# Optimization experiments

Hardware: AMD Instinct MI355X
Metric: run time of the kernel (lower is better)

## Reference

```python
import jax, jax.numpy as jnp
import numpy as np

N = 256
NH = 256  # GRU hidden units
K = 2     # local Hilbert space dim (hardcoded in module)


def gru_step(x, h, Wk, Wr, b):
    # TF keras GRU, reset_after=True, gate order (z, r, h)
    gx = x @ Wk + b[0]          # [B, 3*NH]
    gh = h @ Wr + b[1]          # [B, 3*NH]
    xz, xr, xh = jnp.split(gx, 3, axis=-1)
    hz, hr, hn = jnp.split(gh, 3, axis=-1)
    z = jax.nn.sigmoid(xz + hz)
    r = jax.nn.sigmoid(xr + hr)
    hh = jnp.tanh(xh + r * hn)
    return z * h + (1.0 - z) * hh


def setup_inputs() -> dict:
    key = jax.random.key(0)
    k1, k2, k3 = jax.random.split(key, 3)
    return {
        "gru_kernel": jax.random.normal(k1, (K, 3 * NH), jnp.float32) * 0.05,
        "gru_rec_kernel": jax.random.normal(k2, (NH, 3 * NH), jnp.float32) * 0.05,
        "gru_bias": jnp.zeros((2, 3 * NH), jnp.float32),
        "dense_kernel": jax.random.normal(k3, (NH, K), jnp.float32) * 0.05,
        "dense_bias": jnp.zeros((K,), jnp.float32),
        "nsamples": 2048,
    }


def reference(gru_kernel, gru_rec_kernel, gru_bias, dense_kernel, dense_bias, nsamples):
    keys = jax.random.split(jax.random.key(42), N)
    x0 = jnp.zeros((nsamples, K), jnp.float32)      # 0 * one_hot(0) == zeros
    h0 = jnp.zeros((nsamples, NH), jnp.float32)
    logP0 = jnp.zeros((nsamples,), jnp.float32)

    def step(carry, key):
        x, h, logP = carry
        h = gru_step(x, h, gru_kernel, gru_rec_kernel, gru_bias)
        probs = jax.nn.softmax(h @ dense_kernel + dense_bias, axis=-1)  # [B, K]
        log_probs = jnp.log(1e-10 + probs)
        s = jax.random.categorical(key, log_probs, axis=-1)             # [B]
        onehot = jax.nn.one_hot(s, K, dtype=jnp.float32)
        logP = logP + jnp.sum(log_probs * onehot, axis=1)
        return (onehot, h, logP), s

    (_, _, logP), samples = jax.lax.scan(step, (x0, h0, logP0), keys)
    samples = samples.T.astype(jnp.int32)  # [nsamples, N]
    return samples, logP
```

## Files before the change

### kernel.cpp

```cpp
#include <hip/hip_runtime.h>
#include <stdint.h>

#define NSTEPS 256
#define NHID   256
#define NG     768
#define BPB    8
#define TPB    768
#define NSAMP  2048

__device__ __forceinline__ uint32_t rotl32(uint32_t v, int r){ return (v<<r)|(v>>(32-r)); }

__device__ __forceinline__ void tf2x32(uint32_t k0, uint32_t k1,
                                       uint32_t x0, uint32_t x1,
                                       uint32_t& o0, uint32_t& o1){
  const uint32_t ks2 = k0 ^ k1 ^ 0x1BD11BDAu;
  x0 += k0; x1 += k1;
#define TF_R(r) { x0 += x1; x1 = rotl32(x1,(r)); x1 ^= x0; }
  TF_R(13) TF_R(15) TF_R(26) TF_R(6)
  x0 += k1;  x1 += ks2 + 1u;
  TF_R(17) TF_R(29) TF_R(16) TF_R(24)
  x0 += ks2; x1 += k0 + 2u;
  TF_R(13) TF_R(15) TF_R(26) TF_R(6)
  x0 += k0;  x1 += k1 + 3u;
  TF_R(17) TF_R(29) TF_R(16) TF_R(24)
  x0 += k1;  x1 += ks2 + 4u;
  TF_R(13) TF_R(15) TF_R(26) TF_R(6)
  x0 += ks2; x1 += k0 + 5u;
#undef TF_R
  o0 = x0; o1 = x1;
}

__device__ __forceinline__ float tanh_xla(float x){
  float xc = fminf(fmaxf(x, -9.0f), 9.0f);
  float x2 = xc*xc;
  float p = -2.76076847742355e-16f;
  p = fmaf(p, x2, 2.00018790482477e-13f);
  p = fmaf(p, x2, -8.60467152213735e-11f);
  p = fmaf(p, x2, 5.12229709037114e-08f);
  p = fmaf(p, x2, 1.48572235717979e-05f);
  p = fmaf(p, x2, 6.37261928875436e-04f);
  p = fmaf(p, x2, 4.89352455891786e-03f);
  p = p * xc;
  float q = 1.19825839466702e-06f;
  q = fmaf(q, x2, 1.18534705686654e-04f);
  q = fmaf(q, x2, 2.26843463243900e-03f);
  q = fmaf(q, x2, 4.89352518554385e-03f);
  float r = p / q;
  return (fabsf(x) < 0.0004f) ? x : r;
}

__device__ __forceinline__ float sigmoid_ref(float x){
  return fmaf(0.5f, tanh_xla(0.5f*x), 0.5f);
}

__device__ __forceinline__ void gfma(float4 h, float4 w0, float4 w1, float4 w2, float4 w3, float4& a){
  a.x = fmaf(h.x, w0.x, a.x); a.y = fmaf(h.x, w0.y, a.y);
  a.z = fmaf(h.x, w0.z, a.z); a.w = fmaf(h.x, w0.w, a.w);
  a.x = fmaf(h.y, w1.x, a.x); a.y = fmaf(h.y, w1.y, a.y);
  a.z = fmaf(h.y, w1.z, a.z); a.w = fmaf(h.y, w1.w, a.w);
  a.x = fmaf(h.z, w2.x, a.x); a.y = fmaf(h.z, w2.y, a.y);
  a.z = fmaf(h.z, w2.z, a.z); a.w = fmaf(h.z, w2.w, a.w);
  a.x = fmaf(h.w, w3.x, a.x); a.y = fmaf(h.w, w3.y, a.y);
  a.z = fmaf(h.w, w3.z, a.z); a.w = fmaf(h.w, w3.w, a.w);
}

__global__ __launch_bounds__(TPB, 3) void rnn_sampler(
    const float* __restrict__ Wk,
    const float* __restrict__ Wr,
    const float* __restrict__ Bias,
    const float* __restrict__ Dk,
    const float* __restrict__ Db,
    float* __restrict__ out)
{
  __shared__ float    h_lds[BPB][NHID];
  __shared__ float    part[4][BPB][NG];
  __shared__ uint32_t key0[NSTEPS];
  __shared__ uint32_t key1[NSTEPS];
  __shared__ float    wk_lds[2*NG];
  __shared__ float    bias_lds[2*NG];
  __shared__ float    dk_lds[NHID*2];
  __shared__ float    db_lds[2];
  __shared__ int      xsel[BPB];
  __shared__ float    logPs[BPB];

  const int tid  = threadIdx.x;
  const int b    = blockIdx.x;
  const int ks   = tid / 192;
  const int cq   = tid % 192;
  const int wid  = tid >> 6;
  const int lane = tid & 63;

  if (tid < NSTEPS) {
    uint32_t o0, o1;
    tf2x32(0u, 42u, 0u, (uint32_t)tid, o0, o1);
    key0[tid] = o0; key1[tid] = o1;
  }
  for (int i = tid; i < BPB*NHID; i += TPB) (&h_lds[0][0])[i] = 0.0f;
  for (int i = tid; i < 2*NG; i += TPB) { wk_lds[i] = Wk[i]; bias_lds[i] = Bias[i]; }
  for (int i = tid; i < NHID*2; i += TPB) dk_lds[i] = Dk[i];
  if (tid < 2) db_lds[tid] = Db[tid];
  if (tid < BPB) { xsel[tid] = 0; logPs[tid] = 0.0f; }
  __syncthreads();

  const int k0 = ks * 64;
  const float* wp = Wr + (size_t)k0 * NG + 4*cq;

  float4 acc[BPB];

  for (int t = 0; t <= NSTEPS; ++t) {
    if (t > 0 && wid < BPB) {
      const int tc = t - 1;
      const int s  = wid;
      float4 h4 = *(const float4*)&h_lds[s][lane * 4];
      float4 d0 = *(const float4*)&dk_lds[lane * 8];
      float4 d1 = *(const float4*)&dk_lds[lane * 8 + 4];
      float a0 = h4.x*d0.x + h4.y*d0.z + h4.z*d1.x + h4.w*d1.z;
      float a1 = h4.x*d0.y + h4.y*d0.w + h4.z*d1.y + h4.w*d1.w;
#pragma unroll
      for (int off = 32; off > 0; off >>= 1) {
        a0 += __shfl_down(a0, off);
        a1 += __shfl_down(a1, off);
      }
      float gv = 0.0f;
      if (lane < 2) {
        const int i = b * BPB + s;
        uint32_t o0, o1;
        tf2x32(key0[tc], key1[tc], 0u, (uint32_t)(2*i + lane), o0, o1);
        uint32_t bits = o0 ^ o1;
        const float TINY = 1.17549435e-38f;
        float u = __uint_as_float((bits >> 9) | 0x3f800000u) - 1.0f;
        u = fmaxf(TINY, u * (1.0f - TINY) + TINY);
        gv = -logf(-logf(u));
      }
      float g1 = __shfl(gv, 1);
      if (lane == 0) {
        float l0 = a0 + db_lds[0], l1 = a1 + db_lds[1];
        float m  = fmaxf(l0, l1);
        float e0 = expf(l0 - m), e1 = expf(l1 - m);
        float sum = e0 + e1;
        float p0 = e0 / sum, p1 = e1 / sum;
        float lp0 = logf(1e-10f + p0), lp1 = logf(1e-10f + p1);
        float v0 = gv + lp0, v1 = g1 + lp1;
        int st = (v1 > v0) ? 1 : 0;
        logPs[s] += st ? lp1 : lp0;
        xsel[s] = 1 + st;
        const int i = b * BPB + s;
        out[(size_t)i * NSTEPS + tc] = (float)st;
      }
    }
    if (t == NSTEPS) break;

#pragma unroll
    for (int s = 0; s < BPB; ++s) acc[s] = make_float4(0.f, 0.f, 0.f, 0.f);

#pragma unroll 2
    for (int g = 0; g < 16; ++g) {
      const float* rp = wp + (size_t)(4*g) * NG;
      float4 w0 = *(const float4*)(rp);
      float4 w1 = *(const float4*)(rp + NG);
      float4 w2 = *(const float4*)(rp + 2*NG);
      float4 w3 = *(const float4*)(rp + 3*NG);
#pragma unroll
      for (int s = 0; s < BPB; ++s) {
        float4 h4 = *(const float4*)&h_lds[s][k0 + 4*g];
        gfma(h4, w0, w1, w2, w3, acc[s]);
      }
    }

#pragma unroll
    for (int s = 0; s < BPB; ++s)
      *(float4*)&part[ks][s][4*cq] = acc[s];
    __syncthreads();

    if (tid < 512) {
      const int s = tid >> 6;
      const int n = (tid & 63) << 2;
      float4 pz0 = *(const float4*)&part[0][s][n];
      float4 pz2 = *(const float4*)&part[2][s][n];
      float4 pz1 = *(const float4*)&part[1][s][n];
      float4 pz3 = *(const float4*)&part[3][s][n];
      float4 pr0 = *(const float4*)&part[0][s][n+256];
      float4 pr2 = *(const float4*)&part[2][s][n+256];
      float4 pr1 = *(const float4*)&part[1][s][n+256];
      float4 pr3 = *(const float4*)&part[3][s][n+256];
      float4 pn0 = *(const float4*)&part[0][s][n+512];
      float4 pn2 = *(const float4*)&part[2][s][n+512];
      float4 pn1 = *(const float4*)&part[1][s][n+512];
      float4 pn3 = *(const float4*)&part[3][s][n+512];
      float4 bhz = *(const float4*)&bias_lds[NG + n];
      float4 bhr = *(const float4*)&bias_lds[NG + n + 256];
      float4 bhn = *(const float4*)&bias_lds[NG + n + 512];
      float4 gxz = *(const float4*)&bias_lds[n];
      float4 gxr = *(const float4*)&bias_lds[n + 256];
      float4 gxh = *(const float4*)&bias_lds[n + 512];
      const int xs = xsel[s];
      if (xs != 0) {
        const float* wkrow = wk_lds + (xs - 1) * NG;
        float4 w0 = *(const float4*)&wkrow[n];
        float4 w1 = *(const float4*)&wkrow[n + 256];
        float4 w2 = *(const float4*)&wkrow[n + 512];
        gxz.x = w0.x + gxz.x; gxz.y = w0.y + gxz.y; gxz.z = w0.z + gxz.z; gxz.w = w0.w + gxz.w;
        gxr.x = w1.x + gxr.x; gxr.y = w1.y + gxr.y; gxr.z = w1.z + gxr.z; gxr.w = w1.w + gxr.w;
        gxh.x = w2.x + gxh.x; gxh.y = w2.y + gxh.y; gxh.z = w2.z + gxh.z; gxh.w = w2.w + gxh.w;
      }
      float4 ho = *(const float4*)&h_lds[s][n];
      float4 hnew;
#define GCOMP(c) { \
      float ghz = ((pz0.c + pz2.c) + (pz1.c + pz3.c)) + bhz.c; \
      float ghr = ((pr0.c + pr2.c) + (pr1.c + pr3.c)) + bhr.c; \
      float ghn = ((pn0.c + pn2.c) + (pn1.c + pn3.c)) + bhn.c; \
      float zg = sigmoid_ref(gxz.c + ghz); \
      float rg = sigmoid_ref(gxr.c + ghr); \
      float hh = tanh_xla(gxh.c + rg * ghn); \
      hnew.c = zg * ho.c + (1.0f - zg) * hh; }
      GCOMP(x) GCOMP(y) GCOMP(z) GCOMP(w)
#undef GCOMP
      *(float4*)&h_lds[s][n] = hnew;
    }
    __syncthreads();
  }

  __syncthreads();

  if (tid < BPB) {
    const int i = b * BPB + tid;
    out[(size_t)NSAMP * NSTEPS + i] = logPs[tid];
  }
}

extern "C" void kernel_launch(void* const* d_in, const int* in_sizes, int n_in,
                              void* d_out, int out_size, void* d_ws, size_t ws_size,
                              hipStream_t stream) {
  const float* Wk = (const float*)d_in[0];
  const float* Wr = (const float*)d_in[1];
  const float* B  = (const float*)d_in[2];
  const float* Dk = (const float*)d_in[3];
  const float* Db = (const float*)d_in[4];
  float* out = (float*)d_out;
  rnn_sampler<<<dim3(NSAMP / BPB), dim3(TPB), 0, stream>>>(Wk, Wr, B, Dk, Db, out);
}
```

Measured before the change: 3.377 ms.

## Halve threads per block and give each thread eight output columns

Drops the block from 768 to 384 threads, so each thread now computes 8 gate columns instead of 4 for all 8 samples. Each h value read from LDS now feeds 8 FMAs, which raises register reuse and cuts LDS reads per FMA. The sampling head now runs on 6 wavefronts, two of which handle two samples each, and the gate update loops over the work in strides. The cost is more registers per thread (64 accumulators), fewer waves to hide the global weight loads, and launch_bounds has been removed.

New measurement: 4.439 ms. +31.5%, slower.

```diff
diff --git a/kernel.cpp b/kernel.cpp
--- a/kernel.cpp
+++ b/kernel.cpp
@@ -5,7 +5,7 @@
 #define NHID   256
 #define NG     768
 #define BPB    8
-#define TPB    768
+#define TPB    384
 #define NSAMP  2048
 
 __device__ __forceinline__ uint32_t rotl32(uint32_t v, int r){ return (v<<r)|(v>>(32-r)); }
@@ -53,18 +53,14 @@
   return fmaf(0.5f, tanh_xla(0.5f*x), 0.5f);
 }
 
-__device__ __forceinline__ void gfma(float4 h, float4 w0, float4 w1, float4 w2, float4 w3, float4& a){
-  a.x = fmaf(h.x, w0.x, a.x); a.y = fmaf(h.x, w0.y, a.y);
-  a.z = fmaf(h.x, w0.z, a.z); a.w = fmaf(h.x, w0.w, a.w);
-  a.x = fmaf(h.y, w1.x, a.x); a.y = fmaf(h.y, w1.y, a.y);
-  a.z = fmaf(h.y, w1.z, a.z); a.w = fmaf(h.y, w1.w, a.w);
-  a.x = fmaf(h.z, w2.x, a.x); a.y = fmaf(h.z, w2.y, a.y);
-  a.z = fmaf(h.z, w2.z, a.z); a.w = fmaf(h.z, w2.w, a.w);
-  a.x = fmaf(h.w, w3.x, a.x); a.y = fmaf(h.w, w3.y, a.y);
-  a.z = fmaf(h.w, w3.z, a.z); a.w = fmaf(h.w, w3.w, a.w);
-}
-
-__global__ __launch_bounds__(TPB, 3) void rnn_sampler(
+__device__ __forceinline__ void fma8(float hc, float4 wa, float4 wb, float4& a0, float4& a1){
+  a0.x = fmaf(hc, wa.x, a0.x); a0.y = fmaf(hc, wa.y, a0.y);
+  a0.z = fmaf(hc, wa.z, a0.z); a0.w = fmaf(hc, wa.w, a0.w);
+  a1.x = fmaf(hc, wb.x, a1.x); a1.y = fmaf(hc, wb.y, a1.y);
+  a1.z = fmaf(hc, wb.z, a1.z); a1.w = fmaf(hc, wb.w, a1.w);
+}
+
+__global__ void rnn_sampler(
     const float* __restrict__ Wk,
     const float* __restrict__ Wr,
     const float* __restrict__ Bias,
@@ -85,8 +81,8 @@
 
   const int tid  = threadIdx.x;
   const int b    = blockIdx.x;
-  const int ks   = tid / 192;
-  const int cq   = tid % 192;
+  const int ks   = tid / 96;
+  const int co   = tid % 96;
   const int wid  = tid >> 6;
   const int lane = tid & 63;
 
@@ -103,78 +99,94 @@
   __syncthreads();
 
   const int k0 = ks * 64;
-  const float* wp = Wr + (size_t)k0 * NG + 4*cq;
-
-  float4 acc[BPB];
+  const float* wp = Wr + (size_t)k0 * NG + 8*co;
+
+  float4 acc[BPB][2];
 
   for (int t = 0; t <= NSTEPS; ++t) {
-    if (t > 0 && wid < BPB) {
+    if (t > 0 && wid < 6) {
       const int tc = t - 1;
-      const int s  = wid;
-      float4 h4 = *(const float4*)&h_lds[s][lane * 4];
-      float4 d0 = *(const float4*)&dk_lds[lane * 8];
-      float4 d1 = *(const float4*)&dk_lds[lane * 8 + 4];
-      float a0 = h4.x*d0.x + h4.y*d0.z + h4.z*d1.x + h4.w*d1.z;
-      float a1 = h4.x*d0.y + h4.y*d0.w + h4.z*d1.y + h4.w*d1.w;
-#pragma unroll
-      for (int off = 32; off > 0; off >>= 1) {
-        a0 += __shfl_down(a0, off);
-        a1 += __shfl_down(a1, off);
+      const int nr = (wid < 4) ? 1 : 2;
+      for (int r = 0; r < nr; ++r) {
+        const int s = (r == 0) ? wid : wid + 2;
+        float4 h4 = *(const float4*)&h_lds[s][lane * 4];
+        float4 d0 = *(const float4*)&dk_lds[lane * 8];
+        float4 d1 = *(const float4*)&dk_lds[lane * 8 + 4];
+        float a0 = h4.x*d0.x + h4.y*d0.z + h4.z*d1.x + h4.w*d1.z;
+        float a1 = h4.x*d0.y + h4.y*d0.w + h4.z*d1.y + h4.w*d1.w;
+#pragma unroll
+        for (int off = 32; off > 0; off >>= 1) {
+          a0 += __shfl_down(a0, off);
+          a1 += __shfl_down(a1, off);
+        }
+        float gv = 0.0f;
+        if (lane < 2) {
+          const int i = b * BPB + s;
+          uint32_t o0, o1;
+          tf2x32(key0[tc], key1[tc], 0u, (uint32_t)(2*i + lane), o0, o1);
+          uint32_t bits = o0 ^ o1;
+          const float TINY = 1.17549435e-38f;
+          float u = __uint_as_float((bits >> 9) | 0x3f800000u) - 1.0f;
+          u = fmaxf(TINY, u * (1.0f - TINY) + TINY);
+          gv = -logf(-logf(u));
+        }
+        float g1 = __shfl(gv, 1);
+        if (lane == 0) {
+          float l0 = a0 + db_lds[0], l1 = a1 + db_lds[1];
+          float m  = fmaxf(l0, l1);
+          float e0 = expf(l0 - m), e1 = expf(l1 - m);
+          float sum = e0 + e1;
+          float p0 = e0 / sum, p1 = e1 / sum;
+          float lp0 = logf(1e-10f + p0), lp1 = logf(1e-10f + p1);
+          float v0 = gv + lp0, v1 = g1 + lp1;
+          int st = (v1 > v0) ? 1 : 0;
+          logPs[s] += st ? lp1 : lp0;
+          xsel[s] = 1 + st;
+          const int i = b * BPB + s;
+          out[(size_t)i * NSTEPS + tc] = (float)st;
+        }
       }
-      float gv = 0.0f;
-      if (lane < 2) {
-        const int i = b * BPB + s;
-        uint32_t o0, o1;
-        tf2x32(key0[tc], key1[tc], 0u, (uint32_t)(2*i + lane), o0, o1);
-        uint32_t bits = o0 ^ o1;
-        const float TINY = 1.17549435e-38f;
-        float u = __uint_as_float((bits >> 9) | 0x3f800000u) - 1.0f;
-        u = fmaxf(TINY, u * (1.0f - TINY) + TINY);
-        gv = -logf(-logf(u));
-      }
-      float g1 = __shfl(gv, 1);
-      if (lane == 0) {
-        float l0 = a0 + db_lds[0], l1 = a1 + db_lds[1];
-        float m  = fmaxf(l0, l1);
-        float e0 = expf(l0 - m), e1 = expf(l1 - m);
-        float sum = e0 + e1;
-        float p0 = e0 / sum, p1 = e1 / sum;
-        float lp0 = logf(1e-10f + p0), lp1 = logf(1e-10f + p1);
-        float v0 = gv + lp0, v1 = g1 + lp1;
-        int st = (v1 > v0) ? 1 : 0;
-        logPs[s] += st ? lp1 : lp0;
-        xsel[s] = 1 + st;
-        const int i = b * BPB + s;
-        out[(size_t)i * NSTEPS + tc] = (float)st;
-      }
     }
     if (t == NSTEPS) break;
 
 #pragma unroll
-    for (int s = 0; s < BPB; ++s) acc[s] = make_float4(0.f, 0.f, 0.f, 0.f);
-
-#pragma unroll 2
+    for (int s = 0; s < BPB; ++s) {
+      acc[s][0] = make_float4(0.f, 0.f, 0.f, 0.f);
+      acc[s][1] = make_float4(0.f, 0.f, 0.f, 0.f);
+    }
+
+    const float* rp = wp;
+#pragma unroll 1
     for (int g = 0; g < 16; ++g) {
-      const float* rp = wp + (size_t)(4*g) * NG;
-      float4 w0 = *(const float4*)(rp);
-      float4 w1 = *(const float4*)(rp + NG);
-      float4 w2 = *(const float4*)(rp + 2*NG);
-      float4 w3 = *(const float4*)(rp + 3*NG);
+      float4 w0a = *(const float4*)(rp);
+      float4 w0b = *(const float4*)(rp + 4);
+      float4 w1a = *(const float4*)(rp + NG);
+      float4 w1b = *(const float4*)(rp + NG + 4);
+      float4 w2a = *(const float4*)(rp + 2*NG);
+      float4 w2b = *(const float4*)(rp + 2*NG + 4);
+      float4 w3a = *(const float4*)(rp + 3*NG);
+      float4 w3b = *(const float4*)(rp + 3*NG + 4);
+      rp += 4 * NG;
 #pragma unroll
       for (int s = 0; s < BPB; ++s) {
         float4 h4 = *(const float4*)&h_lds[s][k0 + 4*g];
-        gfma(h4, w0, w1, w2, w3, acc[s]);
+        fma8(h4.x, w0a, w0b, acc[s][0], acc[s][1]);
+        fma8(h4.y, w1a, w1b, acc[s][0], acc[s][1]);
+        fma8(h4.z, w2a, w2b, acc[s][0], acc[s][1]);
+        fma8(h4.w, w3a, w3b, acc[s][0], acc[s][1]);
       }
     }
 
 #pragma unroll
-    for (int s = 0; s < BPB; ++s)
-      *(float4*)&part[ks][s][4*cq] = acc[s];
+    for (int s = 0; s < BPB; ++s) {
+      *(float4*)&part[ks][s][8*co]     = acc[s][0];
+      *(float4*)&part[ks][s][8*co + 4] = acc[s][1];
+    }
     __syncthreads();
 
-    if (tid < 512) {
-      const int s = tid >> 6;
-      const int n = (tid & 63) << 2;
+    for (int it = tid; it < 512; it += TPB) {
+      const int s = it >> 6;
+      const int n = (it & 63) << 2;
       float4 pz0 = *(const float4*)&part[0][s][n];
       float4 pz2 = *(const float4*)&part[2][s][n];
       float4 pz1 = *(const float4*)&part[1][s][n];
```
